# Kernel tuning notes

Hardware: AMD Instinct MI355X
Metric: run time of the kernel (lower is better)

Reference implementation:

```python
import jax, jax.numpy as jnp
import numpy as np

B, IN_UNIT, C, U, OUT = 256, 8, 1152, 10, 16  # batch, input_unit, input_channels, num_unit, unit_size
NUM_ROUTES = 4


def squash(s, axis):
    # norm_sqr/(1+norm_sqr) * s/||s||, matching the torch squash (no eps, as in source)
    n2 = jnp.sum(s * s, axis=axis, keepdims=True)
    return n2 / (1.0 + n2) * (s / jnp.sqrt(n2))


def setup_inputs() -> dict:
    key = jax.random.key(0)
    k1, k2 = jax.random.split(key)
    x = jax.random.normal(k1, (B, IN_UNIT, C), dtype=jnp.float32)
    W = jax.random.normal(k2, (C, U, OUT, IN_UNIT), dtype=jnp.float32)  # torch weights squeezed of leading 1
    return {"x": x, "W": W}


def reference(x, W):
    # x: [B, in_unit, C] -> [B, C, in_unit]
    xt = jnp.transpose(x, (0, 2, 1))
    # predict_vectors u_hat[b,c,u,:] = W[c,u] @ x[b,c]  -> [B, C, U, OUT]
    u_hat = jnp.einsum('bci,cuoi->bcuo', xt, W)
    b = jnp.zeros((C, U), dtype=x.dtype)  # routing logits (torch: [1,C,U,1] zeros)
    v = None
    for _ in range(NUM_ROUTES):
        c = jax.nn.softmax(b, axis=1)                      # softmax over num_unit (dim=2 in torch layout)
        s = jnp.einsum('cu,bcuo->buo', c, u_hat)           # weighted sum over input capsules -> [B,U,OUT]
        v = squash(s, axis=2)                              # squash over unit_size dim
        agreement = jnp.einsum('bcuo,buo->bcu', u_hat, v)  # u_hat^T v, -> [B,C,U]
        b = b + jnp.mean(agreement, axis=0)                # mean over batch, as in source
    return v[..., None]  # [B, U, OUT, 1] matching vec_out.squeeze(1)
```

## Files before the change

kernel.cpp:

```cpp
#include <hip/hip_runtime.h>
#include <cstdint>
#include <cstddef>

typedef _Float16 half_t;
typedef __attribute__((ext_vector_type(8))) _Float16 f16x8;
typedef __attribute__((ext_vector_type(4))) _Float16 f16x4;
typedef __attribute__((ext_vector_type(4))) float f32x4;
typedef unsigned int uint_t;
typedef unsigned short ushort_t;

#define OFF_W1   0
#define OFF_WD   2949120
#define OFF_XHF  8847360
#define OFF_XKH  13565952
#define OFF_VHF  18284544
#define OFF_AG   18366464
#define WS_NEED  18642944

__device__ __forceinline__ void gload16(const void* g, void* l) {
  __builtin_amdgcn_global_load_lds(
      (const __attribute__((address_space(1))) unsigned int*)g,
      (__attribute__((address_space(3))) unsigned int*)l, 16, 0, 0);
}

__global__ void k_setup(const float* __restrict__ x, const float* __restrict__ W,
                        half_t* __restrict__ w1, float* __restrict__ wd,
                        half_t* __restrict__ xhf, half_t* __restrict__ xkh) {
  int bid = blockIdx.x, tid = threadIdx.x;
  if (bid < 720) {
    int gid = bid * 256 + tid;
    int ll = gid & 63, tile = gid >> 6;
    int nt = tile % 10, kt = tile / 10;
    int lmm = ll & 15, lgg = ll >> 4;
    f16x8 o;
#pragma unroll
    for (int j = 0; j < 8; ++j) {
      int k = kt * 32 + lgg * 8 + j;
      int i = k / 1152, c = k - i * 1152;
      o[j] = (half_t)W[((size_t)(c * 10 + nt) * 16 + lmm) * 8 + i];
    }
    *(f16x8*)(w1 + (size_t)gid * 8) = o;
  } else if (bid < 2160) {
    int g2 = (bid - 720) * 256 + tid;
    int ll = g2 & 63, tile = g2 >> 6;
    int nt = tile % 10, mt2 = tile / 10;
    int lmm = ll & 15, lgg = ll >> 4;
    float vv[4];
#pragma unroll
    for (int r = 0; r < 4; ++r) {
      int krow = mt2 * 16 + lgg * 4 + r;
      int i = krow / 1152, c = krow - i * 1152;
      vv[r] = W[((size_t)(c * 10 + nt) * 16 + lmm) * 8 + i];
    }
    *(float4*)(wd + (size_t)g2 * 4) = make_float4(vv[0], vv[1], vv[2], vv[3]);
  } else if (bid < 3312) {
    int t = (bid - 2160) * 256 + tid;
    const float4 a0 = *(const float4*)(x + (size_t)t * 8);
    const float4 a1 = *(const float4*)(x + (size_t)t * 8 + 4);
    f16x8 o;
    o[0] = (half_t)a0.x; o[1] = (half_t)a0.y; o[2] = (half_t)a0.z; o[3] = (half_t)a0.w;
    o[4] = (half_t)a1.x; o[5] = (half_t)a1.y; o[6] = (half_t)a1.z; o[7] = (half_t)a1.w;
    *(f16x8*)(xhf + (size_t)t * 8) = o;
  } else {
    __shared__ float sh[32 * 33];
    int tb = bid - 3312;
    int k0 = (tb % 288) * 32, b0 = (tb / 288) * 32;
    int tx = tid & 31, ty = tid >> 5;
#pragma unroll
    for (int r = 0; r < 32; r += 8)
      sh[(ty + r) * 33 + tx] = x[(size_t)(b0 + ty + r) * 9216 + k0 + tx];
    __syncthreads();
#pragma unroll
    for (int r = 0; r < 32; r += 8)
      xkh[(size_t)(k0 + ty + r) * 256 + b0 + tx] = (half_t)sh[tx * 33 + ty + r];
  }
}

__global__ __launch_bounds__(1024) void k_g1sq(const half_t* __restrict__ xhf,
                                               const half_t* __restrict__ w1,
                                               const float* __restrict__ ag,
                                               half_t* __restrict__ vhfT,
                                               float* __restrict__ out, int it) {
  int mb = blockIdx.x, nt = blockIdx.y;
  int tid = threadIdx.x;
  int wv = tid >> 6, l = tid & 63, lm = l & 15, lgp = l >> 4;
  __shared__ __align__(16) half_t cwf[1152];
  __shared__ __align__(16) half_t stage[16][3][2][512];
  __shared__ __align__(16) float red[16][64][4];

  for (int c = tid; c < 1152; c += 1024) {
    float lv[10] = {0.f, 0.f, 0.f, 0.f, 0.f, 0.f, 0.f, 0.f, 0.f, 0.f};
    for (int t = 0; t < it; ++t)
#pragma unroll
      for (int bty = 0; bty < 2; ++bty) {
        const float* a = ag + ((size_t)(t * 2 + bty) * 10) * 1152 + c;
#pragma unroll
        for (int u = 0; u < 10; ++u) lv[u] += a[(size_t)u * 1152];
      }
    float mx = lv[0];
#pragma unroll
    for (int u = 1; u < 10; ++u) mx = fmaxf(mx, lv[u]);
    float ssum = 0.f, sel = 0.f;
#pragma unroll
    for (int u = 0; u < 10; ++u) {
      float e = __expf((lv[u] - mx) * (1.0f / 256.0f));
      ssum += e;
      if (u == nt) sel = e;
    }
    cwf[c] = (half_t)(sel / ssum);
  }
  __syncthreads();

  const half_t* xbase = xhf + (size_t)(mb * 16 + (l >> 2)) * 9216 + (l & 3) * 8;
  int kt0 = wv * 18;
  int ktc0 = (wv & 1) * 18;
#define ISSUE(J)                                                                     \
  do {                                                                               \
    int kt_ = kt0 + (J);                                                             \
    gload16(xbase + (size_t)kt_ * 32, &stage[wv][(J) % 3][0][0]);                    \
    gload16(w1 + ((size_t)(kt_ * 10 + nt) * 512) + l * 8, &stage[wv][(J) % 3][1][0]);\
  } while (0)

  ISSUE(0);
  ISSUE(1);
  ISSUE(2);

  f32x4 acc0 = {0.f, 0.f, 0.f, 0.f};
  f32x4 acc1 = {0.f, 0.f, 0.f, 0.f};
#pragma unroll
  for (int j = 0; j < 18; ++j) {
    const int buf = j % 3;
    if (j <= 15) {
      asm volatile("s_waitcnt vmcnt(4)" ::: "memory");
    } else if (j == 16) {
      asm volatile("s_waitcnt vmcnt(2)" ::: "memory");
    } else {
      asm volatile("s_waitcnt vmcnt(0)" ::: "memory");
    }
    __builtin_amdgcn_sched_barrier(0);
    f16x8 af = *(const f16x8*)&stage[wv][buf][0][lm * 32 + lgp * 8];
    f16x8 wf = *(const f16x8*)&stage[wv][buf][1][l * 8];
    f16x8 cwk = *(const f16x8*)(&cwf[(ktc0 + j) * 32 + lgp * 8]);
    if ((j & 1) == 0) acc0 = __builtin_amdgcn_mfma_f32_16x16x32_f16(af, wf * cwk, acc0, 0, 0, 0);
    else              acc1 = __builtin_amdgcn_mfma_f32_16x16x32_f16(af, wf * cwk, acc1, 0, 0, 0);
    __builtin_amdgcn_sched_barrier(0);
    if (j + 3 < 18) ISSUE(j + 3);
    __builtin_amdgcn_sched_barrier(0);
  }
#undef ISSUE
  acc0[0] += acc1[0]; acc0[1] += acc1[1]; acc0[2] += acc1[2]; acc0[3] += acc1[3];
  *(f32x4*)&red[wv][l][0] = acc0;
  __syncthreads();
  if (wv == 0) {
    float4 s = make_float4(0.f, 0.f, 0.f, 0.f);
#pragma unroll
    for (int w = 0; w < 16; ++w) {
      s.x += red[w][l][0]; s.y += red[w][l][1];
      s.z += red[w][l][2]; s.w += red[w][l][3];
    }
    float4 n2 = make_float4(s.x * s.x, s.y * s.y, s.z * s.z, s.w * s.w);
#pragma unroll
    for (int off = 1; off < 16; off <<= 1) {
      n2.x += __shfl_xor(n2.x, off);
      n2.y += __shfl_xor(n2.y, off);
      n2.z += __shfl_xor(n2.z, off);
      n2.w += __shfl_xor(n2.w, off);
    }
    float4 vv;
    vv.x = s.x * (n2.x / ((1.f + n2.x) * sqrtf(n2.x)));
    vv.y = s.y * (n2.y / ((1.f + n2.y) * sqrtf(n2.y)));
    vv.z = s.z * (n2.z / ((1.f + n2.z) * sqrtf(n2.z)));
    vv.w = s.w * (n2.w / ((1.f + n2.w) * sqrtf(n2.w)));
    if (it == 3) {
      float* ob = out + (size_t)(mb * 16 + lgp * 4) * 160 + nt * 16 + lm;
      ob[0 * 160] = vv.x; ob[1 * 160] = vv.y; ob[2 * 160] = vv.z; ob[3 * 160] = vv.w;
    } else {
      f16x4 h;
      h[0] = (half_t)vv.x; h[1] = (half_t)vv.y; h[2] = (half_t)vv.z; h[3] = (half_t)vv.w;
      *(f16x4*)(vhfT + (size_t)(nt * 16 + lm) * 256 + mb * 16 + lgp * 4) = h;
    }
  }
}

__global__ __launch_bounds__(512) void k_g2(const half_t* __restrict__ xkh,
                                            const half_t* __restrict__ vhfT,
                                            const float* __restrict__ wd,
                                            float* __restrict__ ag, int it) {
  int cb = blockIdx.x, bty = blockIdx.y;
  int tid = threadIdx.x;
  int wv = tid >> 6, l = tid & 63, lm = l & 15, lgp = l >> 4;
  int mt = wv * 72 + cb;
  __shared__ float red2[8][16][10];

  f32x4 z = {0.f, 0.f, 0.f, 0.f};
  f32x4 acc[10];
#pragma unroll
  for (int nt = 0; nt < 10; ++nt) acc[nt] = z;

#pragma unroll
  for (int bt = 0; bt < 4; ++bt) {
    int btg = bty * 4 + bt;
    f16x8 af = *(const f16x8*)(xkh + (size_t)(mt * 16 + lm) * 256 + btg * 32 + lgp * 8);
#pragma unroll
    for (int nt = 0; nt < 10; ++nt) {
      f16x8 bfr = *(const f16x8*)(vhfT + (size_t)(nt * 16 + lm) * 256 + btg * 32 + lgp * 8);
      acc[nt] = __builtin_amdgcn_mfma_f32_16x16x32_f16(af, bfr, acc[nt], 0, 0, 0);
    }
  }
#pragma unroll
  for (int nt = 0; nt < 10; ++nt) {
    float4 wdv = *(const float4*)(wd + ((size_t)(mt * 10 + nt) * 64 + l) * 4);
    float p0 = acc[nt][0] * wdv.x;
    float p1 = acc[nt][1] * wdv.y;
    float p2 = acc[nt][2] * wdv.z;
    float p3 = acc[nt][3] * wdv.w;
#pragma unroll
    for (int off = 1; off < 16; off <<= 1) {
      p0 += __shfl_xor(p0, off);
      p1 += __shfl_xor(p1, off);
      p2 += __shfl_xor(p2, off);
      p3 += __shfl_xor(p3, off);
    }
    if (lm == 0) {
      red2[wv][lgp * 4 + 0][nt] = p0;
      red2[wv][lgp * 4 + 1][nt] = p1;
      red2[wv][lgp * 4 + 2][nt] = p2;
      red2[wv][lgp * 4 + 3][nt] = p3;
    }
  }
  __syncthreads();
  if (tid < 160) {
    int u = tid >> 4, cc = tid & 15;
    float ss = 0.f;
#pragma unroll
    for (int w = 0; w < 8; ++w) ss += red2[w][cc][u];
    ag[((size_t)(it * 2 + bty) * 10 + u) * 1152 + cb * 16 + cc] = ss;
  }
}

extern "C" void kernel_launch(void* const* d_in, const int* in_sizes, int n_in,
                              void* d_out, int out_size, void* d_ws, size_t ws_size,
                              hipStream_t stream) {
  const float* x = (const float*)d_in[0];
  const float* W = (const float*)d_in[1];
  float* out = (float*)d_out;
  char* ws = (char*)d_ws;
  if (ws_size < WS_NEED) return;

  half_t* w1  = (half_t*)(ws + OFF_W1);
  float*  wd  = (float*)(ws + OFF_WD);
  half_t* xhf = (half_t*)(ws + OFF_XHF);
  half_t* xkh = (half_t*)(ws + OFF_XKH);
  half_t* vhfT= (half_t*)(ws + OFF_VHF);
  float*  ag  = (float*)(ws + OFF_AG);

  k_setup<<<dim3(5616), dim3(256), 0, stream>>>(x, W, w1, wd, xhf, xkh);
  for (int it = 0; it < 4; ++it) {
    k_g1sq<<<dim3(16, 10), dim3(1024), 0, stream>>>(xhf, w1, ag, vhfT, out, it);
    if (it < 3)
      k_g2<<<dim3(72, 2), dim3(512), 0, stream>>>(xkh, vhfT, wd, ag, it);
  }
}
```

Baseline: 141.1 us.

## Reorder GEMM K dimension to c-major so W converts with a plain cast

Measured after the change: 121.3 us. 14.0% less time.

```diff
diff --git a/kernel.cpp b/kernel.cpp
--- a/kernel.cpp
+++ b/kernel.cpp
@@ -7,15 +7,13 @@
 typedef __attribute__((ext_vector_type(4))) _Float16 f16x4;
 typedef __attribute__((ext_vector_type(4))) float f32x4;
 typedef unsigned int uint_t;
-typedef unsigned short ushort_t;
-
-#define OFF_W1   0
-#define OFF_WD   2949120
-#define OFF_XHF  8847360
-#define OFF_XKH  13565952
-#define OFF_VHF  18284544
-#define OFF_AG   18366464
-#define WS_NEED  18642944
+
+#define OFF_WH   0
+#define OFF_XHF  2949120
+#define OFF_XKH  7667712
+#define OFF_VHF  12386304
+#define OFF_AG   12468224
+#define WS_NEED  12606464
 
 __device__ __forceinline__ void gload16(const void* g, void* l) {
   __builtin_amdgcn_global_load_lds(
@@ -24,60 +22,57 @@
 }
 
 __global__ void k_setup(const float* __restrict__ x, const float* __restrict__ W,
-                        half_t* __restrict__ w1, float* __restrict__ wd,
-                        half_t* __restrict__ xhf, half_t* __restrict__ xkh) {
+                        half_t* __restrict__ wh, half_t* __restrict__ xhf,
+                        half_t* __restrict__ xkh) {
   int bid = blockIdx.x, tid = threadIdx.x;
   if (bid < 720) {
     int gid = bid * 256 + tid;
-    int ll = gid & 63, tile = gid >> 6;
-    int nt = tile % 10, kt = tile / 10;
-    int lmm = ll & 15, lgg = ll >> 4;
-    f16x8 o;
-#pragma unroll
-    for (int j = 0; j < 8; ++j) {
-      int k = kt * 32 + lgg * 8 + j;
-      int i = k / 1152, c = k - i * 1152;
-      o[j] = (half_t)W[((size_t)(c * 10 + nt) * 16 + lmm) * 8 + i];
-    }
-    *(f16x8*)(w1 + (size_t)gid * 8) = o;
-  } else if (bid < 2160) {
-    int g2 = (bid - 720) * 256 + tid;
-    int ll = g2 & 63, tile = g2 >> 6;
-    int nt = tile % 10, mt2 = tile / 10;
-    int lmm = ll & 15, lgg = ll >> 4;
-    float vv[4];
-#pragma unroll
-    for (int r = 0; r < 4; ++r) {
-      int krow = mt2 * 16 + lgg * 4 + r;
-      int i = krow / 1152, c = krow - i * 1152;
-      vv[r] = W[((size_t)(c * 10 + nt) * 16 + lmm) * 8 + i];
-    }
-    *(float4*)(wd + (size_t)g2 * 4) = make_float4(vv[0], vv[1], vv[2], vv[3]);
-  } else if (bid < 3312) {
-    int t = (bid - 2160) * 256 + tid;
-    const float4 a0 = *(const float4*)(x + (size_t)t * 8);
-    const float4 a1 = *(const float4*)(x + (size_t)t * 8 + 4);
+    const float4 a0 = *(const float4*)(W + (size_t)gid * 8);
+    const float4 a1 = *(const float4*)(W + (size_t)gid * 8 + 4);
     f16x8 o;
     o[0] = (half_t)a0.x; o[1] = (half_t)a0.y; o[2] = (half_t)a0.z; o[3] = (half_t)a0.w;
     o[4] = (half_t)a1.x; o[5] = (half_t)a1.y; o[6] = (half_t)a1.z; o[7] = (half_t)a1.w;
-    *(f16x8*)(xhf + (size_t)t * 8) = o;
+    *(f16x8*)(wh + (size_t)gid * 8) = o;
+  } else if (bid < 976) {
+    int b = bid - 720;
+    __shared__ float lds_f[9216];
+    const float4* xr = (const float4*)(x + (size_t)b * 9216);
+    for (int t = tid; t < 2304; t += 256) {
+      float4 v = xr[t];
+      lds_f[t * 4 + 0] = v.x; lds_f[t * 4 + 1] = v.y;
+      lds_f[t * 4 + 2] = v.z; lds_f[t * 4 + 3] = v.w;
+    }
+    __syncthreads();
+    for (int t = tid; t < 1152; t += 256) {
+      f16x8 o;
+#pragma unroll
+      for (int i = 0; i < 8; ++i) o[i] = (half_t)lds_f[i * 1152 + t];
+      *(f16x8*)(xhf + (size_t)b * 9216 + t * 8) = o;
+    }
   } else {
-    __shared__ float sh[32 * 33];
-    int tb = bid - 3312;
-    int k0 = (tb % 288) * 32, b0 = (tb / 288) * 32;
-    int tx = tid & 31, ty = tid >> 5;
-#pragma unroll
-    for (int r = 0; r < 32; r += 8)
-      sh[(ty + r) * 33 + tx] = x[(size_t)(b0 + ty + r) * 9216 + k0 + tx];
+    int tb = bid - 976;
+    int kt = tb % 288, bt = tb / 288;
+    int c0 = kt * 4, b0 = bt * 32;
+    __shared__ float lt[32][36];
+    int bl = tid >> 3, ch = tid & 7;
+    float4 v = *(const float4*)(x + (size_t)(b0 + bl) * 9216 + ch * 1152 + c0);
+    lt[bl][0 * 8 + ch] = v.x;
+    lt[bl][1 * 8 + ch] = v.y;
+    lt[bl][2 * 8 + ch] = v.z;
+    lt[bl][3 * 8 + ch] = v.w;
     __syncthreads();
-#pragma unroll
-    for (int r = 0; r < 32; r += 8)
-      xkh[(size_t)(k0 + ty + r) * 256 + b0 + tx] = (half_t)sh[tx * 33 + ty + r];
+    int kl = tid >> 3, bg = tid & 7;
+    f16x4 h;
+    h[0] = (half_t)lt[bg * 4 + 0][kl];
+    h[1] = (half_t)lt[bg * 4 + 1][kl];
+    h[2] = (half_t)lt[bg * 4 + 2][kl];
+    h[3] = (half_t)lt[bg * 4 + 3][kl];
+    *(f16x4*)(xkh + (size_t)(kt * 32 + kl) * 256 + b0 + bg * 4) = h;
   }
 }
 
 __global__ __launch_bounds__(1024) void k_g1sq(const half_t* __restrict__ xhf,
-                                               const half_t* __restrict__ w1,
+                                               const half_t* __restrict__ wh,
                                                const float* __restrict__ ag,
                                                half_t* __restrict__ vhfT,
                                                float* __restrict__ out, int it) {
@@ -92,11 +87,7 @@
     float lv[10] = {0.f, 0.f, 0.f, 0.f, 0.f, 0.f, 0.f, 0.f, 0.f, 0.f};
     for (int t = 0; t < it; ++t)
 #pragma unroll
-      for (int bty = 0; bty < 2; ++bty) {
-        const float* a = ag + ((size_t)(t * 2 + bty) * 10) * 1152 + c;
-#pragma unroll
-        for (int u = 0; u < 10; ++u) lv[u] += a[(size_t)u * 1152];
-      }
+      for (int u = 0; u < 10; ++u) lv[u] += ag[(size_t)(t * 10 + u) * 1152 + c];
     float mx = lv[0];
 #pragma unroll
     for (int u = 1; u < 10; ++u) mx = fmaxf(mx, lv[u]);
@@ -112,13 +103,14 @@
   __syncthreads();
 
   const half_t* xbase = xhf + (size_t)(mb * 16 + (l >> 2)) * 9216 + (l & 3) * 8;
+  const half_t* wbase = wh + ((size_t)(lgp * 10 + nt) * 16 + lm) * 8;
   int kt0 = wv * 18;
-  int ktc0 = (wv & 1) * 18;
-#define ISSUE(J)                                                                     \
-  do {                                                                               \
-    int kt_ = kt0 + (J);                                                             \
-    gload16(xbase + (size_t)kt_ * 32, &stage[wv][(J) % 3][0][0]);                    \
-    gload16(w1 + ((size_t)(kt_ * 10 + nt) * 512) + l * 8, &stage[wv][(J) % 3][1][0]);\
+  int cbase = kt0 * 4 + lgp;
+#define ISSUE(J)                                                                   \
+  do {                                                                             \
+    int kt_ = kt0 + (J);                                                           \
+    gload16(xbase + (size_t)kt_ * 32, &stage[wv][(J) % 3][0][0]);                  \
+    gload16(wbase + (size_t)kt_ * 5120, &stage[wv][(J) % 3][1][0]);                \
   } while (0)
 
   ISSUE(0);
@@ -140,9 +132,10 @@
     __builtin_amdgcn_sched_barrier(0);
     f16x8 af = *(const f16x8*)&stage[wv][buf][0][lm * 32 + lgp * 8];
     f16x8 wf = *(const f16x8*)&stage[wv][buf][1][l * 8];
-    f16x8 cwk = *(const f16x8*)(&cwf[(ktc0 + j) * 32 + lgp * 8]);
-    if ((j & 1) == 0) acc0 = __builtin_amdgcn_mfma_f32_16x16x32_f16(af, wf * cwk, acc0, 0, 0, 0);
-    else              acc1 = __builtin_amdgcn_mfma_f32_16x16x32_f16(af, wf * cwk, acc1, 0, 0, 0);
+    half_t sc = cwf[cbase + j * 4];
+    f16x8 bsc = wf * sc;
+    if ((j & 1) == 0) acc0 = __builtin_amdgcn_mfma_f32_16x16x32_f16(af, bsc, acc0, 0, 0, 0);
+    else              acc1 = __builtin_amdgcn_mfma_f32_16x16x32_f16(af, bsc, acc1, 0, 0, 0);
     __builtin_amdgcn_sched_barrier(0);
     if (j + 3 < 18) ISSUE(j + 3);
     __builtin_amdgcn_sched_barrier(0);
@@ -182,59 +175,43 @@
   }
 }
 
-__global__ __launch_bounds__(512) void k_g2(const half_t* __restrict__ xkh,
+__global__ __launch_bounds__(256) void k_g2(const half_t* __restrict__ xkh,
                                             const half_t* __restrict__ vhfT,
-                                            const float* __restrict__ wd,
+                                            const float* __restrict__ W,
                                             float* __restrict__ ag, int it) {
-  int cb = blockIdx.x, bty = blockIdx.y;
+  int cb = blockIdx.x;
   int tid = threadIdx.x;
   int wv = tid >> 6, l = tid & 63, lm = l & 15, lgp = l >> 4;
-  int mt = wv * 72 + cb;
-  __shared__ float red2[8][16][10];
-
+  int mt = cb * 4 + wv;
   f32x4 z = {0.f, 0.f, 0.f, 0.f};
   f32x4 acc[10];
 #pragma unroll
   for (int nt = 0; nt < 10; ++nt) acc[nt] = z;
 
 #pragma unroll
-  for (int bt = 0; bt < 4; ++bt) {
-    int btg = bty * 4 + bt;
-    f16x8 af = *(const f16x8*)(xkh + (size_t)(mt * 16 + lm) * 256 + btg * 32 + lgp * 8);
+  for (int bt = 0; bt < 8; ++bt) {
+    f16x8 af = *(const f16x8*)(xkh + (size_t)(mt * 16 + lm) * 256 + bt * 32 + lgp * 8);
 #pragma unroll
     for (int nt = 0; nt < 10; ++nt) {
-      f16x8 bfr = *(const f16x8*)(vhfT + (size_t)(nt * 16 + lm) * 256 + btg * 32 + lgp * 8);
+      f16x8 bfr = *(const f16x8*)(vhfT + (size_t)(nt * 16 + lm) * 256 + bt * 32 + lgp * 8);
       acc[nt] = __builtin_amdgcn_mfma_f32_16x16x32_f16(af, bfr, acc[nt], 0, 0, 0);
     }
   }
+  int cc = mt * 2 + (lgp >> 1);
+  int i0 = (lgp & 1) * 4;
+  float* agt = ag + (size_t)it * 11520;
 #pragma unroll
   for (int nt = 0; nt < 10; ++nt) {
-    float4 wdv = *(const float4*)(wd + ((size_t)(mt * 10 + nt) * 64 + l) * 4);
-    float p0 = acc[nt][0] * wdv.x;
-    float p1 = acc[nt][1] * wdv.y;
-    float p2 = acc[nt][2] * wdv.z;
-    float p3 = acc[nt][3] * wdv.w;
-#pragma unroll
-    for (int off = 1; off < 16; off <<= 1) {
-      p0 += __shfl_xor(p0, off);
-      p1 += __shfl_xor(p1, off);
-      p2 += __shfl_xor(p2, off);
-      p3 += __shfl_xor(p3, off);
-    }
-    if (lm == 0) {
-      red2[wv][lgp * 4 + 0][nt] = p0;
-      red2[wv][lgp * 4 + 1][nt] = p1;
-      red2[wv][lgp * 4 + 2][nt] = p2;
-      red2[wv][lgp * 4 + 3][nt] = p3;
-    }
-  }
-  __syncthreads();
-  if (tid < 160) {
-    int u = tid >> 4, cc = tid & 15;
-    float ss = 0.f;
-#pragma unroll
-    for (int w = 0; w < 8; ++w) ss += red2[w][cc][u];
-    ag[((size_t)(it * 2 + bty) * 10 + u) * 1152 + cb * 16 + cc] = ss;
+    float4 wdv = *(const float4*)(W + ((size_t)(cc * 10 + nt) * 16 + lm) * 8 + i0);
+    float q = acc[nt][0] * wdv.x + acc[nt][1] * wdv.y
+            + acc[nt][2] * wdv.z + acc[nt][3] * wdv.w;
+    q += __shfl_xor(q, 1);
+    q += __shfl_xor(q, 2);
+    q += __shfl_xor(q, 4);
+    q += __shfl_xor(q, 8);
+    q += __shfl_xor(q, 16);
+    if (lm == 0 && (lgp & 1) == 0)
+      agt[(size_t)nt * 1152 + cc] = q;
   }
 }
 
@@ -247,17 +224,16 @@
   char* ws = (char*)d_ws;
   if (ws_size < WS_NEED) return;
 
-  half_t* w1  = (half_t*)(ws + OFF_W1);
-  float*  wd  = (float*)(ws + OFF_WD);
+  half_t* wh  = (half_t*)(ws + OFF_WH);
   half_t* xhf = (half_t*)(ws + OFF_XHF);
   half_t* xkh = (half_t*)(ws + OFF_XKH);
   half_t* vhfT= (half_t*)(ws + OFF_VHF);
   float*  ag  = (float*)(ws + OFF_AG);
 
-  k_setup<<<dim3(5616), dim3(256), 0, stream>>>(x, W, w1, wd, xhf, xkh);
+  k_setup<<<dim3(3280), dim3(256), 0, stream>>>(x, W, wh, xhf, xkh);
   for (int it = 0; it < 4; ++it) {
-    k_g1sq<<<dim3(16, 10), dim3(1024), 0, stream>>>(xhf, w1, ag, vhfT, out, it);
+    k_g1sq<<<dim3(16, 10), dim3(1024), 0, stream>>>(xhf, wh, ag, vhfT, out, it);
     if (it < 3)
-      k_g2<<<dim3(72, 2), dim3(512), 0, stream>>>(xkh, vhfT, wd, ag, it);
-  }
-}
+      k_g2<<<dim3(144), dim3(256), 0, stream>>>(xkh, vhfT, W, ag, it);
+  }
+}
```
